# Optimization experiments

Hardware: AMD Instinct MI355X
Metric: run time of the kernel (lower is better)

Reference implementation:

```python
import jax, jax.numpy as jnp
import numpy as np

N = 50000
E = 800000
NODE_IN = 64
EDGE_IN = 8
OUT = 1
SAGE_DIMS = [(64, 64), (64, 64), (64, 32), (32, 32)]
EDGE_DIMS = [(8, 64), (64, 64), (64, 32), (32, 32)]


def setup_inputs():
    key = jax.random.key(0)
    keys = iter(jax.random.split(key, 64))
    d = {}
    d["x"] = jax.random.normal(next(keys), (N, NODE_IN), jnp.float32)
    d["dis"] = jax.random.normal(next(keys), (E, EDGE_IN), jnp.float32)
    d["edge_index"] = jax.random.randint(next(keys), (2, E), 0, N, dtype=jnp.int32)
    for i, (fi, fo) in enumerate(SAGE_DIMS):
        d[f"s{i}_wl"] = jax.random.normal(next(keys), (fi, fo), jnp.float32) / np.sqrt(fi).astype(np.float32)
        d[f"s{i}_bl"] = jnp.zeros((fo,), jnp.float32)
        d[f"s{i}_wr"] = jax.random.normal(next(keys), (fi, fo), jnp.float32) / np.sqrt(fi).astype(np.float32)
    for i, (fi, h) in enumerate(EDGE_DIMS):
        d[f"e{i}_w1"] = jax.random.normal(next(keys), (fi, 2 * h), jnp.float32) / np.sqrt(fi).astype(np.float32)
        d[f"e{i}_b1"] = jnp.zeros((2 * h,), jnp.float32)
        d[f"e{i}_w2"] = jax.random.normal(next(keys), (2 * h, h), jnp.float32) / np.sqrt(2 * h).astype(np.float32)
        d[f"e{i}_b2"] = jnp.zeros((h,), jnp.float32)
    d["fc_w"] = jax.random.normal(next(keys), (64, OUT), jnp.float32) / 8.0
    d["fc_b"] = jnp.zeros((OUT,), jnp.float32)
    return d


def _sage(x, row, col, wl, bl, wr):
    # PyG SAGEConv (aggr='mean'): lin_l(mean_{j->i} x_j) + lin_r(x_i); lin_l has bias.
    msg = x[row]  # [E, F] gather of source features
    s = jax.ops.segment_sum(msg, col, num_segments=N)
    cnt = jax.ops.segment_sum(jnp.ones((row.shape[0], 1), x.dtype), col, num_segments=N)
    mean = s / jnp.maximum(cnt, 1.0)  # isolated nodes -> 0 (matches scatter-mean)
    return mean @ wl + bl + x @ wr


def _edge_conv(dis, col, w1, b1, w2, b2):
    # EdgeOnlyConv: add_self_loops with num_nodes=E and zero edge_attr, so the
    # output has E rows; self-loop message = lin(0) = b1 and each segment t gets
    # mean = (sum_{edges->t} lin(dis) + b1) / (deg_in(t) + 1); then lin_update.
    msg = dis @ w1 + b1  # [E, 2h]
    s = jax.ops.segment_sum(msg, col, num_segments=E)
    deg = jax.ops.segment_sum(jnp.ones((col.shape[0], 1), dis.dtype), col, num_segments=E)
    aggr = (s + b1) / (deg + 1.0)
    return aggr @ w2 + b2


def _forward(x, dis, edge_index, sage_params, edge_params, fc_w, fc_b):
    row, col = edge_index[0], edge_index[1]
    h = x
    for wl, bl, wr in sage_params:
        h = jax.nn.leaky_relu(_sage(h, row, col, wl, bl, wr))
    d = dis
    for w1, b1, w2, b2 in edge_params:
        d = jax.nn.leaky_relu(_edge_conv(d, col, w1, b1, w2, b2))
    # dropout is identity at inference
    feats = jnp.concatenate([h[row] * h[col], d], axis=1)  # [E, hidden]
    return feats @ fc_w + fc_b


def reference(x, dis, edge_index, s0_wl, s0_bl, s0_wr, s1_wl, s1_bl, s1_wr, s2_wl, s2_bl, s2_wr, s3_wl, s3_bl, s3_wr, e0_w1, e0_b1, e0_w2, e0_b2, e1_w1, e1_b1, e1_w2, e1_b2, e2_w1, e2_b1, e2_w2, e2_b2, e3_w1, e3_b1, e3_w2, e3_b2, fc_w, fc_b):
    sage_params = [(s0_wl, s0_bl, s0_wr), (s1_wl, s1_bl, s1_wr), (s2_wl, s2_bl, s2_wr), (s3_wl, s3_bl, s3_wr)]
    edge_params = [(e0_w1, e0_b1, e0_w2, e0_b2), (e1_w1, e1_b1, e1_w2, e1_b2), (e2_w1, e2_b1, e2_w2, e2_b2), (e3_w1, e3_b1, e3_w2, e3_b2)]
    return _forward(x, dis, edge_index, sage_params, edge_params, fc_w, fc_b)
```

## Files before the change

kernel.cpp:

```cpp
#include <hip/hip_runtime.h>

#define LRELU(v) ((v) > 0.0f ? (v) : 0.01f * (v))

__device__ __forceinline__ unsigned short f2bf(float f) {
    union { float f; unsigned u; } c;
    c.f = f;
    return (unsigned short)((c.u + 0x7fffu + ((c.u >> 16) & 1)) >> 16);
}
__device__ __forceinline__ float bf_lo(unsigned u) {
    union { unsigned i; float f; } v;
    v.i = u << 16;
    return v.f;
}
__device__ __forceinline__ float bf_hi(unsigned u) {
    union { unsigned i; float f; } v;
    v.i = u & 0xffff0000u;
    return v.f;
}

__global__ void bucket_count_k(const int* __restrict__ col, int* __restrict__ bcnt, int E) {
    __shared__ int lcnt[512];
    int tid = threadIdx.x;
    for (int i = tid; i < 512; i += 1024) lcnt[i] = 0;
    __syncthreads();
    int base = blockIdx.x * 8192;
    for (int k = 0; k < 8; ++k) {
        int e = base + k * 1024 + tid;
        if (e < E) atomicAdd(&lcnt[col[e] >> 7], 1);
    }
    __syncthreads();
    for (int i = tid; i < 512; i += 1024) {
        int v = lcnt[i];
        if (v) atomicAdd(&bcnt[i], v);
    }
}

__global__ void bucket_scan_k(const int* __restrict__ bcnt, int* __restrict__ bbase,
                              int* __restrict__ bwp, int NBUCK, int E) {
    __shared__ int s[512];
    int tid = threadIdx.x;
    int v = (tid < NBUCK) ? bcnt[tid] : 0;
    s[tid] = v;
    __syncthreads();
    for (int off = 1; off < 512; off <<= 1) {
        int t = (tid >= off) ? s[tid - off] : 0;
        __syncthreads();
        s[tid] += t;
        __syncthreads();
    }
    if (tid < NBUCK) {
        int ex = s[tid] - v;
        bbase[tid] = ex;
        bwp[tid] = ex;
    }
    if (tid == 0) bbase[NBUCK] = E;
}

__global__ void bucket_scatter_k(const int* __restrict__ row, const int* __restrict__ col,
                                 int* __restrict__ bwp, int2* __restrict__ tmp, int E) {
    __shared__ int lcnt[512];
    __shared__ int gbase[512];
    int tid = threadIdx.x;
    for (int i = tid; i < 512; i += 1024) lcnt[i] = 0;
    __syncthreads();
    int base = blockIdx.x * 8192;
    int lpos[8], bk[8];
    for (int k = 0; k < 8; ++k) {
        int e = base + k * 1024 + tid;
        if (e < E) {
            int b = col[e] >> 7;
            bk[k] = b;
            lpos[k] = atomicAdd(&lcnt[b], 1);
        } else
            bk[k] = -1;
    }
    __syncthreads();
    for (int i = tid; i < 512; i += 1024) {
        int v = lcnt[i];
        gbase[i] = v ? atomicAdd(&bwp[i], v) : 0;
    }
    __syncthreads();
    for (int k = 0; k < 8; ++k) {
        int e = base + k * 1024 + tid;
        if (e < E) {
            int c = col[e];
            tmp[gbase[bk[k]] + lpos[k]] = make_int2(row[e], ((c & 127) << 25) | e);
        }
    }
}

__global__ void bucket_csr_k(const int2* __restrict__ tmp, const int* __restrict__ bbase,
                             int* __restrict__ rowptr, int* __restrict__ cnt,
                             int* __restrict__ rows, int* __restrict__ eids, int N, int E) {
    constexpr int CAP = 6144;
    __shared__ int2 buf[CAP];
    __shared__ int lcnt[128];
    __shared__ int sscan[128];
    __shared__ int lwp[128];
    int b = blockIdx.x;
    int tid = threadIdx.x;
    int s = bbase[b], e = bbase[b + 1];
    int sz = e - s;
    if (tid < 128) lcnt[tid] = 0;
    __syncthreads();
    for (int i = tid; i < sz; i += 256) {
        int2 v = tmp[s + i];
        if (i < CAP) buf[i] = v;
        atomicAdd(&lcnt[((unsigned)v.y) >> 25], 1);
    }
    __syncthreads();
    if (tid < 128) sscan[tid] = lcnt[tid];
    __syncthreads();
    for (int off = 1; off < 128; off <<= 1) {
        int t = (tid < 128 && tid >= off) ? sscan[tid - off] : 0;
        __syncthreads();
        if (tid < 128) sscan[tid] += t;
        __syncthreads();
    }
    if (tid < 128) {
        int ex = sscan[tid] - lcnt[tid];
        lwp[tid] = ex;
        int c = b * 128 + tid;
        if (c < N) {
            rowptr[c] = s + ex;
            cnt[c] = lcnt[tid];
            if (c == N - 1) rowptr[N] = E;
        }
    }
    __syncthreads();
    for (int i = tid; i < sz; i += 256) {
        int2 v = (i < CAP) ? buf[i] : tmp[s + i];
        int cl = ((unsigned)v.y) >> 25;
        int p = atomicAdd(&lwp[cl], 1);
        rows[s + p] = v.x;
        eids[s + p] = v.y & 0x1FFFFFF;
    }
}

template <int FIN, int FOUT, bool BFL>
__global__ void gemm2_k(const float* __restrict__ h, const float* __restrict__ wl,
                        const float* __restrict__ wr, const float* __restrict__ bl,
                        void* __restrict__ hl, float* __restrict__ hr, int N) {
    constexpr int XT = (2 * FOUT) / 4;
    constexpr int YT = 256 / XT;
    constexpr int NPT = 4;
    constexpr int NPB = YT * NPT;
    __shared__ float sw[FIN * 2 * FOUT];
    int lin = threadIdx.y * XT + threadIdx.x;
    for (int idx = lin; idx < FIN * FOUT; idx += 256) {
        int f = idx / FOUT, o = idx % FOUT;
        sw[f * 2 * FOUT + o] = wl[idx];
        sw[f * 2 * FOUT + FOUT + o] = wr[idx];
    }
    __syncthreads();
    int og = threadIdx.x * 4;
    int base = blockIdx.x * NPB + threadIdx.y * NPT;
    int ix[NPT] = {min(base + 0, N - 1), min(base + 1, N - 1), min(base + 2, N - 1),
                   min(base + 3, N - 1)};
    float4 s[NPT] = {{0.f, 0.f, 0.f, 0.f}, {0.f, 0.f, 0.f, 0.f}, {0.f, 0.f, 0.f, 0.f},
                     {0.f, 0.f, 0.f, 0.f}};
#pragma unroll 2
    for (int f = 0; f < FIN; f += 4) {
        float4 w0 = *(const float4*)&sw[(f + 0) * 2 * FOUT + og];
        float4 w1 = *(const float4*)&sw[(f + 1) * 2 * FOUT + og];
        float4 w2 = *(const float4*)&sw[(f + 2) * 2 * FOUT + og];
        float4 w3 = *(const float4*)&sw[(f + 3) * 2 * FOUT + og];
#pragma unroll
        for (int k = 0; k < NPT; ++k) {
// ... 13 lines not shown
            int i = base + k;
            if (i < N) {
                float4 r = {s[k].x + bias.x, s[k].y + bias.y, s[k].z + bias.z, s[k].w + bias.w};
                *(float4*)(hr + (size_t)i * FOUT + oo) = r;
            }
        }
    } else {
#pragma unroll
        for (int k = 0; k < NPT; ++k) {
            int i = base + k;
            if (i < N) {
                if (BFL) {
                    unsigned short* d = (unsigned short*)hl + (size_t)i * FOUT + oo;
                    *(ushort4*)d =
                        make_ushort4(f2bf(s[k].x), f2bf(s[k].y), f2bf(s[k].z), f2bf(s[k].w));
                } else {
                    *(float4*)((float*)hl + (size_t)i * FOUT + oo) = s[k];
                }
            }
        }
    }
}

__global__ void aggr_fused64_bf_k(const unsigned short* __restrict__ hlb,
                                  const float* __restrict__ hr, const int* __restrict__ rowptr,
                                  const int* __restrict__ rows, float* __restrict__ out, int N) {
    int wave = (blockIdx.x * blockDim.x + threadIdx.x) >> 6;
    int lane = threadIdx.x & 63;
    if (wave >= N) return;
    int u = lane >> 4, f4 = lane & 15;
    int s = rowptr[wave], e = rowptr[wave + 1];
    float4 a = {0.f, 0.f, 0.f, 0.f};
    int p = s + u;
    for (; p + 4 < e; p += 8) {
        int r0 = rows[p], r1 = rows[p + 4];
        uint2 v0 = ((const uint2*)(hlb + (size_t)r0 * 64))[f4];
        uint2 v1 = ((const uint2*)(hlb + (size_t)r1 * 64))[f4];
        a.x += bf_lo(v0.x) + bf_lo(v1.x);
        a.y += bf_hi(v0.x) + bf_hi(v1.x);
        a.z += bf_lo(v0.y) + bf_lo(v1.y);
        a.w += bf_hi(v0.y) + bf_hi(v1.y);
    }
    if (p < e) {
        uint2 v = ((const uint2*)(hlb + (size_t)rows[p] * 64))[f4];
        a.x += bf_lo(v.x); a.y += bf_hi(v.x); a.z += bf_lo(v.y); a.w += bf_hi(v.y);
    }
    a.x += __shfl_down(a.x, 32); a.y += __shfl_down(a.y, 32);
    a.z += __shfl_down(a.z, 32); a.w += __shfl_down(a.w, 32);
    a.x += __shfl_down(a.x, 16); a.y += __shfl_down(a.y, 16);
    a.z += __shfl_down(a.z, 16); a.w += __shfl_down(a.w, 16);
    if (lane < 16) {
        float inv = 1.0f / fmaxf((float)(e - s), 1.0f);
        float4 r = ((const float4*)(hr + (size_t)wave * 64))[f4];
        float4 o;
        o.x = LRELU(a.x * inv + r.x);
        o.y = LRELU(a.y * inv + r.y);
        o.z = LRELU(a.z * inv + r.z);
        o.w = LRELU(a.w * inv + r.w);
        ((float4*)(out + (size_t)wave * 64))[f4] = o;
    }
}

template <bool OUTBF>
__global__ void aggr_fused32_bf_k(const unsigned short* __restrict__ hlb,
                                  const float* __restrict__ hr, const int* __restrict__ rowptr,
                                  const int* __restrict__ rows, void* __restrict__ out, int N) {
    int wave = (blockIdx.x * blockDim.x + threadIdx.x) >> 6;
    int lane = threadIdx.x & 63;
    if (wave >= N) return;
    int u = lane >> 3, f4 = lane & 7;
    int s = rowptr[wave], e = rowptr[wave + 1];
    float4 a = {0.f, 0.f, 0.f, 0.f};
    int p = s + u;
    for (; p + 8 < e; p += 16) {
        int r0 = rows[p], r1 = rows[p + 8];
        uint2 v0 = ((const uint2*)(hlb + (size_t)r0 * 32))[f4];
        uint2 v1 = ((const uint2*)(hlb + (size_t)r1 * 32))[f4];
        a.x += bf_lo(v0.x) + bf_lo(v1.x);
        a.y += bf_hi(v0.x) + bf_hi(v1.x);
        a.z += bf_lo(v0.y) + bf_lo(v1.y);
        a.w += bf_hi(v0.y) + bf_hi(v1.y);
    }
    if (p < e) {
        uint2 v = ((const uint2*)(hlb + (size_t)rows[p] * 32))[f4];
        a.x += bf_lo(v.x); a.y += bf_hi(v.x); a.z += bf_lo(v.y); a.w += bf_hi(v.y);
    }
    a.x += __shfl_down(a.x, 32); a.y += __shfl_down(a.y, 32);
    a.z += __shfl_down(a.z, 32); a.w += __shfl_down(a.w, 32);
    a.x += __shfl_down(a.x, 16); a.y += __shfl_down(a.y, 16);
    a.z += __shfl_down(a.z, 16); a.w += __shfl_down(a.w, 16);
    a.x += __shfl_down(a.x, 8); a.y += __shfl_down(a.y, 8);
    a.z += __shfl_down(a.z, 8); a.w += __shfl_down(a.w, 8);
    if (lane < 8) {
        float inv = 1.0f / fmaxf((float)(e - s), 1.0f);
        const float4* hp = (const float4*)(hr + (size_t)wave * 32);
        float4 r = hp[f4];
        float4 o;
        o.x = LRELU(a.x * inv + r.x);
        o.y = LRELU(a.y * inv + r.y);
        o.z = LRELU(a.z * inv + r.z);
        o.w = LRELU(a.w * inv + r.w);
        if (OUTBF) {
            unsigned short* d = (unsigned short*)out + (size_t)wave * 32 + f4 * 4;
            *(ushort4*)d = make_ushort4(f2bf(o.x), f2bf(o.y), f2bf(o.z), f2bf(o.w));
        } else {
            ((float4*)((float*)out + (size_t)wave * 32))[f4] = o;
        }
    }
}

__global__ void edge_aggr8_k(const float* __restrict__ dis, const int* __restrict__ rowptr,
                             const int* __restrict__ eids, float* __restrict__ sd,
                             float* __restrict__ zbuf, int N) {
    int wave = (blockIdx.x * blockDim.x + threadIdx.x) >> 6;
    int lane = threadIdx.x & 63;
    if (wave >= N) return;
    zbuf[(size_t)wave * 64 + lane] = 0.0f;
    int u = lane >> 1, f4 = lane & 1;
    int s = rowptr[wave], e = rowptr[wave + 1];
    float4 a = {0.f, 0.f, 0.f, 0.f};
    for (int p = s + u; p < e; p += 32) {
        const float4* dp = (const float4*)(dis + (size_t)eids[p] * 8);
        float4 v = dp[f4];
        a.x += v.x; a.y += v.y; a.z += v.z; a.w += v.w;
    }
    for (int off = 32; off >= 2; off >>= 1) {
        a.x += __shfl_down(a.x, off); a.y += __shfl_down(a.y, off);
        a.z += __shfl_down(a.z, off); a.w += __shfl_down(a.w, off);
    }
    if (lane < 2) ((float4*)(sd + (size_t)wave * 8))[f4] = a;
}

template <int H2, int HOUT>
__device__ __forceinline__ void w12_body(const float* __restrict__ w1,
                                         const float* __restrict__ w2, float* __restrict__ out,
                                         int i, int o) {
    float s = 0.0f;
#pragma unroll
    for (int k = 0; k < H2; ++k) s += w1[i * H2 + k] * w2[k * HOUT + o];
    out[i * HOUT + o] = s;
}

__global__ void w12c_k(const float* __restrict__ w1_0, const float* __restrict__ w2_0,
                       float* __restrict__ o0, const float* __restrict__ w1_1,
                       const float* __restrict__ w2_1, float* __restrict__ o1,
                       const float* __restrict__ w1_2, const float* __restrict__ w2_2,
                       float* __restrict__ o2, const float* __restrict__ w1_3,
                       const float* __restrict__ w2_3, float* __restrict__ o3,
                       const float* __restrict__ b1_0, const float* __restrict__ b2_0,
                       const float* __restrict__ b1_1, const float* __restrict__ b2_1,
                       const float* __restrict__ b1_2, const float* __restrict__ b2_2,
                       const float* __restrict__ b1_3, const float* __restrict__ b2_3,
                       float* cbuf, int* __restrict__ bcnt) {
    int b = blockIdx.x;
    int o = threadIdx.x;
    if (b < 8) {
        if (o < 64) w12_body<128, 64>(w1_0, w2_0, o0, b, o);
    } else if (b < 72) {
        if (o < 64) w12_body<128, 64>(w1_1, w2_1, o1, b - 8, o);
    } else if (b < 136) {
        if (o < 32) w12_body<64, 32>(w1_2, w2_2, o2, b - 72, o);
    } else if (b < 168) {
        if (o < 32) w12_body<64, 32>(w1_3, w2_3, o3, b - 136, o);
    } else if (b == 168) {
        __shared__ float c1[64], c2[64], c3[32], u1[128], u2[64], u3[64];
        float t;
        if (o < 64) {
            t = 0.0f;
#pragma unroll
            for (int k = 0; k < 128; ++k) t += b1_0[k] * w2_0[k * 64 + o];
            cbuf[192 + o] = t;
            c1[o] = LRELU(t + b2_0[o]);
            cbuf[o] = c1[o];
            t = 0.0f;
#pragma unroll
            for (int k = 0; k < 128; ++k) t += b1_1[k] * w2_1[k * 64 + o];
            cbuf[256 + o] = t;
            c2[o] = LRELU(t + b2_1[o]);
            cbuf[64 + o] = c2[o];
        }
        if (o < 32) {
            t = 0.0f;
#pragma unroll
            for (int k = 0; k < 64; ++k) t += b1_2[k] * w2_2[k * 32 + o];
            cbuf[384 + o] = t;
            c3[o] = LRELU(t + b2_2[o]);
            cbuf[128 + o] = c3[o];
            t = 0.0f;
#pragma unroll
            for (int k = 0; k < 64; ++k) t += b1_3[k] * w2_3[k * 32 + o];
            cbuf[448 + o] = t;
            cbuf[160 + o] = LRELU(t + b2_3[o]);
        }
        __syncthreads();
        {
            float s = 0.0f;
#pragma unroll
            for (int f = 0; f < 64; ++f) s += c1[f] * w1_1[f * 128 + o];
            u1[o] = s;
        }
        if (o < 64) {
            float s = 0.0f;
#pragma unroll
            for (int f = 0; f < 64; ++f) s += c2[f] * w1_2[f * 64 + o];
            u2[o] = s;
            float s3 = 0.0f;
#pragma unroll
            for (int f = 0; f < 32; ++f) s3 += c3[f] * w1_3[f * 64 + o];
            u3[o] = s3;
        }
        __syncthreads();
        if (o < 64) {
            float s = cbuf[256 + o];
#pragma unroll
            for (int k = 0; k < 128; ++k) s += u1[k] * w2_1[k * 64 + o];
            cbuf[320 + o] = s;
        }
        if (o < 32) {
            float s = cbuf[384 + o];
#pragma unroll
            for (int k = 0; k < 64; ++k) s += u2[k] * w2_2[k * 32 + o];
            cbuf[416 + o] = s;
            float s3 = cbuf[448 + o];
#pragma unroll
            for (int k = 0; k < 64; ++k) s3 += u3[k] * w2_3[k * 32 + o];
            cbuf[480 + o] = s3;
        }
    } else {
        bcnt[o] = 0; bcnt[o + 128] = 0; bcnt[o + 256] = 0; bcnt[o + 384] = 0;
    }
}

template <int FIN, int FOUT>
__global__ void edge_compute_scatter_k(const float* __restrict__ sd, const int* __restrict__ cnt,
                                       const float* __restrict__ w12, const float* __restrict__ mw2,
                                       const float* __restrict__ b1w2, const float* __restrict__ b2,
                                       const float* __restrict__ cnext,
                                       const int* __restrict__ col, float* __restrict__ sdnext,
                                       int N, float* __restrict__ zbuf, int zf4) {
    constexpr int ROWS = 256 / FOUT;
    constexpr int NPT = 4;
    constexpr int NPB = ROWS * NPT;
    __shared__ float sw[FIN * FOUT];
    int lin = threadIdx.y * FOUT + threadIdx.x;
    for (int idx = lin; idx < FIN * FOUT; idx += 256) sw[idx] = w12[idx];
    __syncthreads();
    if (zf4) {
        float4 z4 = {0.f, 0.f, 0.f, 0.f};
        for (int z = blockIdx.x * 256 + lin; z < zf4; z += gridDim.x * 256)
            ((float4*)zbuf)[z] = z4;
    }
    int o = threadIdx.x;
    int base = blockIdx.x * NPB + threadIdx.y * NPT;
    int ix[NPT] = {min(base + 0, N - 1), min(base + 1, N - 1), min(base + 2, N - 1),
                   min(base + 3, N - 1)};
    float s[NPT] = {0.f, 0.f, 0.f, 0.f};
#pragma unroll 2
    for (int f = 0; f < FIN; f += 4) {
        float w0 = sw[(f + 0) * FOUT + o], w1 = sw[(f + 1) * FOUT + o];
        float w2 = sw[(f + 2) * FOUT + o], w3 = sw[(f + 3) * FOUT + o];
#pragma unroll
        for (int k = 0; k < NPT; ++k) {
// ... 25 lines not shown
    int lin = threadIdx.y * FOUT + threadIdx.x;
    for (int idx = lin; idx < FIN * FOUT; idx += 256) sw[idx] = w12[idx];
    __syncthreads();
    int o = threadIdx.x;
    int base = blockIdx.x * NPB + threadIdx.y * NPT;
    int ix[NPT] = {min(base + 0, N - 1), min(base + 1, N - 1), min(base + 2, N - 1),
                   min(base + 3, N - 1)};
    float s[NPT] = {0.f, 0.f, 0.f, 0.f};
#pragma unroll 2
    for (int f = 0; f < FIN; f += 4) {
        float w0 = sw[(f + 0) * FOUT + o], w1 = sw[(f + 1) * FOUT + o];
        float w2 = sw[(f + 2) * FOUT + o], w3 = sw[(f + 3) * FOUT + o];
#pragma unroll
        for (int k = 0; k < NPT; ++k) {
            float4 v = *(const float4*)(sd + (size_t)ix[k] * FIN + f);
            s[k] += v.x * w0 + v.y * w1 + v.z * w2 + v.w * w3;
        }
    }
    float mo = mw2[o], bo = b1w2[o], b2o = b2[o], fw = fcw[32 + o];
#pragma unroll
    for (int k = 0; k < NPT; ++k) {
        float deg = (float)cnt[ix[k]];
        float inv = 1.0f / (deg + 1.0f);
        float v = LRELU((s[k] + deg * mo + bo) * inv + b2o) * fw;
        v += __shfl_down(v, 16);
        v += __shfl_down(v, 8);
        v += __shfl_down(v, 4);
        v += __shfl_down(v, 2);
        v += __shfl_down(v, 1);
        if (o == 0 && base + k < N) ddot[base + k] = v;
    }
}

__device__ __forceinline__ float bdot8(uint4 a, uint4 b, const float* __restrict__ w) {
    return bf_lo(a.x) * bf_lo(b.x) * w[0] + bf_hi(a.x) * bf_hi(b.x) * w[1] +
           bf_lo(a.y) * bf_lo(b.y) * w[2] + bf_hi(a.y) * bf_hi(b.y) * w[3] +
           bf_lo(a.z) * bf_lo(b.z) * w[4] + bf_hi(a.z) * bf_hi(b.z) * w[5] +
           bf_lo(a.w) * bf_lo(b.w) * w[6] + bf_hi(a.w) * bf_hi(b.w) * w[7];
}

__global__ void final_k(const unsigned short* __restrict__ h3b, const float* __restrict__ ddot,
                        const float* __restrict__ c4, const int* __restrict__ row,
                        const int* __restrict__ col, const float* __restrict__ fcw,
                        const float* __restrict__ fcb, float* __restrict__ out, int E, int N) {
    __shared__ float sw[64];
    __shared__ float sc4[32];
    __shared__ float cdot_s;
    int tid = threadIdx.x;
    if (tid < 64) sw[tid] = fcw[tid];
    if (tid < 32) sc4[tid] = c4[tid];
    __syncthreads();
    if (tid == 0) {
        float cd = 0.0f;
#pragma unroll
        for (int k = 0; k < 32; ++k) cd += sc4[k] * sw[32 + k];
        cdot_s = cd;
    }
    __syncthreads();
    float fb = fcb[0];
    float cdot = cdot_s;
    int e0 = blockIdx.x * 512 + tid;
    int e1 = e0 + 256;
    bool v0 = e0 < E, v1 = e1 < E;
    int r0 = 0, c0 = 0, r1 = 0, c1 = 0;
    if (v0) { r0 = row[e0]; c0 = col[e0]; }
    if (v1) { r1 = row[e1]; c1 = col[e1]; }
    uint4 a00, a01, b00, b01, a10, a11, b10, b11;
    if (v0) {
        const uint4* pr = (const uint4*)(h3b + (size_t)r0 * 32);
        const uint4* pc = (const uint4*)(h3b + (size_t)c0 * 32);
        a00 = pr[0]; a01 = pr[1]; b00 = pc[0]; b01 = pc[1];
    }
    if (v1) {
        const uint4* pr = (const uint4*)(h3b + (size_t)r1 * 32);
        const uint4* pc = (const uint4*)(h3b + (size_t)c1 * 32);
        a10 = pr[0]; a11 = pr[1]; b10 = pc[0]; b11 = pc[1];
    }
    if (v0) {
        float s = fb + bdot8(a00, b00, sw) + bdot8(a01, b01, sw + 8) +
                  bdot8(((const uint4*)(h3b + (size_t)r0 * 32))[2],
                        ((const uint4*)(h3b + (size_t)c0 * 32))[2], sw + 16) +
                  bdot8(((const uint4*)(h3b + (size_t)r0 * 32))[3],
                        ((const uint4*)(h3b + (size_t)c0 * 32))[3], sw + 24);
        s += (e0 < N) ? ddot[e0] : cdot;
        out[e0] = s;
    }
    if (v1) {
        float s = fb + bdot8(a10, b10, sw) + bdot8(a11, b11, sw + 8) +
                  bdot8(((const uint4*)(h3b + (size_t)r1 * 32))[2],
                        ((const uint4*)(h3b + (size_t)c1 * 32))[2], sw + 16) +
                  bdot8(((const uint4*)(h3b + (size_t)r1 * 32))[3],
                        ((const uint4*)(h3b + (size_t)c1 * 32))[3], sw + 24);
        s += (e1 < N) ? ddot[e1] : cdot;
        out[e1] = s;
    }
}

extern "C" void kernel_launch(void* const* d_in, const int* in_sizes, int n_in, void* d_out,
                              int out_size, void* d_ws, size_t ws_size, hipStream_t stream) {
    const float* x = (const float*)d_in[0];
    const float* dis = (const float*)d_in[1];
    const int* ei = (const int*)d_in[2];
    const float* s_wl[4] = {(const float*)d_in[3], (const float*)d_in[6], (const float*)d_in[9],
                            (const float*)d_in[12]};
    const float* s_bl[4] = {(const float*)d_in[4], (const float*)d_in[7], (const float*)d_in[10],
                            (const float*)d_in[13]};
    const float* s_wr[4] = {(const float*)d_in[5], (const float*)d_in[8], (const float*)d_in[11],
                            (const float*)d_in[14]};
    const float* e_w1[4] = {(const float*)d_in[15], (const float*)d_in[19], (const float*)d_in[23],
                            (const float*)d_in[27]};
    const float* e_b1[4] = {(const float*)d_in[16], (const float*)d_in[20], (const float*)d_in[24],
                            (const float*)d_in[28]};
    const float* e_w2[4] = {(const float*)d_in[17], (const float*)d_in[21], (const float*)d_in[25],
                            (const float*)d_in[29]};
    const float* e_b2[4] = {(const float*)d_in[18], (const float*)d_in[22], (const float*)d_in[26],
                            (const float*)d_in[30]};
    const float* fcw = (const float*)d_in[31];
    const float* fcb = (const float*)d_in[32];

    const int N = in_sizes[0] / 64;
    const int E = in_sizes[1] / 8;
    const int* row = ei;
    const int* col = ei + E;
    const int NBUCK = (N + 127) / 128;
    const int EB = (E + 8191) / 8192;

    auto au = [](size_t v) { return (v + 255) & ~(size_t)255; };
    char* p = (char*)d_ws;
    int* cnt = (int*)p;       p += au((size_t)N * 4);
    int* rowptr = (int*)p;    p += au((size_t)(N + 1) * 4);
    int* bcnt = (int*)p;      p += au(512 * 4);
    int* bbase = (int*)p;     p += au(513 * 4);
    int* bwp = (int*)p;       p += au(512 * 4);
    float* w12_0 = (float*)p; p += au(512 * 4);
    float* w12_1 = (float*)p; p += au(4096 * 4);
    float* w12_2 = (float*)p; p += au(2048 * 4);
    float* w12_3 = (float*)p; p += au(1024 * 4);
    float* cbuf = (float*)p;  p += au(512 * 4);
    int* rowsA = (int*)p;     p += au((size_t)E * 4);
    int* eidsA = (int*)p;     p += au((size_t)E * 4);
    float* acc = (float*)p;   p += au((size_t)N * 64 * 4);
    float* hA = (float*)p;    p += au((size_t)N * 64 * 4);
    float* hB = (float*)p;    p += au((size_t)N * 64 * 4);
    float* dvA = (float*)p;   p += au((size_t)N * 64 * 4);
    float* dvB = (float*)p;   p += au((size_t)N * 64 * 4);

    int2* tmp = (int2*)dvA;
    unsigned short* hlb = (unsigned short*)acc;
    unsigned short* h3b = (unsigned short*)hA;
    float* ddot = dvB;

    w12c_k<<<170, 128, 0, stream>>>(e_w1[0], e_w2[0], w12_0, e_w1[1], e_w2[1], w12_1, e_w1[2],
                                    e_w2[2], w12_2, e_w1[3], e_w2[3], w12_3, e_b1[0], e_b2[0],
                                    e_b1[1], e_b2[1], e_b1[2], e_b2[2], e_b1[3], e_b2[3], cbuf,
                                    bcnt);

    bucket_count_k<<<EB, 1024, 0, stream>>>(col, bcnt, E);
    bucket_scan_k<<<1, 512, 0, stream>>>(bcnt, bbase, bwp, NBUCK, E);
    bucket_scatter_k<<<EB, 1024, 0, stream>>>(row, col, bwp, tmp, E);
    bucket_csr_k<<<NBUCK, 256, 0, stream>>>(tmp, bbase, rowptr, cnt, rowsA, eidsA, N, E);

    const int WPB = 4;

    gemm2_k<64, 64, true><<<(N + 31) / 32, dim3(32, 8), 0, stream>>>(x, s_wl[0], s_wr[0], s_bl[0],
                                                                     hlb, dvB, N);
    aggr_fused64_bf_k<<<(N + WPB - 1) / WPB, 256, 0, stream>>>(hlb, dvB, rowptr, rowsA, hA, N);
    gemm2_k<64, 64, true><<<(N + 31) / 32, dim3(32, 8), 0, stream>>>(hA, s_wl[1], s_wr[1], s_bl[1],
                                                                     hlb, dvB, N);
    aggr_fused64_bf_k<<<(N + WPB - 1) / WPB, 256, 0, stream>>>(hlb, dvB, rowptr, rowsA, hB, N);
    gemm2_k<64, 32, true><<<(N + 63) / 64, dim3(16, 16), 0, stream>>>(hB, s_wl[2], s_wr[2],
                                                                      s_bl[2], hlb, dvB, N);
    aggr_fused32_bf_k<false><<<(N + WPB - 1) / WPB, 256, 0, stream>>>(hlb, dvB, rowptr, rowsA, hA,
                                                                      N);
    gemm2_k<32, 32, true><<<(N + 63) / 64, dim3(16, 16), 0, stream>>>(hA, s_wl[3], s_wr[3],
                                                                      s_bl[3], hlb, dvB, N);
    aggr_fused32_bf_k<true><<<(N + WPB - 1) / WPB, 256, 0, stream>>>(hlb, dvB, rowptr, rowsA, h3b,
                                                                     N);

    edge_aggr8_k<<<(N + WPB - 1) / WPB, 256, 0, stream>>>(dis, rowptr, eidsA, hB, dvA, N);
    edge_compute_scatter_k<8, 64><<<(N + 15) / 16, dim3(64, 4), 0, stream>>>(
        hB, cnt, w12_0, cbuf + 192, cbuf + 192, e_b2[0], cbuf + 0, col, dvA, N, acc, N * 16);
    edge_compute_scatter_k<64, 64><<<(N + 15) / 16, dim3(64, 4), 0, stream>>>(
        dvA, cnt, w12_1, cbuf + 320, cbuf + 256, e_b2[1], cbuf + 64, col, acc, N, hB, N * 8);
    edge_compute_scatter_k<64, 32><<<(N + 31) / 32, dim3(32, 8), 0, stream>>>(
        acc, cnt, w12_2, cbuf + 416, cbuf + 384, e_b2[2], cbuf + 128, col, hB, N, nullptr, 0);
    edge_dot_k<<<(N + 31) / 32, dim3(32, 8), 0, stream>>>(hB, cnt, w12_3, cbuf + 480, cbuf + 448,
                                                          e_b2[3], fcw, ddot, N);

    final_k<<<(E + 511) / 512, 256, 0, stream>>>(h3b, ddot, cbuf + 160, row, col, fcw, fcb,
                                                 (float*)d_out, E, N);
}
```

Baseline: 467.2 us.

## Merge setup kernels, fuse CSR build with first GEMM, and make final pass CSR-driven

Folds the weight-precompute kernel into the bucket-count kernel, using per-block partial counts instead of global atomics. The CSR build and the first SAGE GEMM now run in one launch through a shared-memory union. The last aggregation is co-launched with the edge-feature aggregation. The final edge scoring walks the CSR per destination node, loading the destination embedding once and computing the source-side dot with the collapsed fc weights. A wider unroll is added to the 64-wide aggregation. These cut launch count and redundant gathers, but add scattered output writes in the final pass and a serial reduction in the scan.

New measurement: 477.3 us. 2.2% more time.

```diff
diff --git a/kernel.cpp b/kernel.cpp
--- a/kernel.cpp
+++ b/kernel.cpp
@@ -18,28 +18,136 @@
     return v.f;
 }
 
-__global__ void bucket_count_k(const int* __restrict__ col, int* __restrict__ bcnt, int E) {
-    __shared__ int lcnt[512];
+template <int H2, int HOUT>
+__device__ __forceinline__ void w12_body(const float* __restrict__ w1,
+                                         const float* __restrict__ w2, float* __restrict__ out,
+                                         int i, int o) {
+    float s = 0.0f;
+#pragma unroll
+    for (int k = 0; k < H2; ++k) s += w1[i * H2 + k] * w2[k * HOUT + o];
+    out[i * HOUT + o] = s;
+}
+
+__global__ void count_w12c_k(const int* __restrict__ col, int* __restrict__ bpart, int E, int EB,
+                             const float* __restrict__ w1_0, const float* __restrict__ w2_0,
+                             float* __restrict__ o0, const float* __restrict__ w1_1,
+                             const float* __restrict__ w2_1, float* __restrict__ o1,
+                             const float* __restrict__ w1_2, const float* __restrict__ w2_2,
+                             float* __restrict__ o2, const float* __restrict__ w1_3,
+                             const float* __restrict__ w2_3, float* __restrict__ o3,
+                             const float* __restrict__ b1_0, const float* __restrict__ b2_0,
+                             const float* __restrict__ b1_1, const float* __restrict__ b2_1,
+                             const float* __restrict__ b1_2, const float* __restrict__ b2_2,
+                             const float* __restrict__ b1_3, const float* __restrict__ b2_3,
+                             const float* __restrict__ fcw, float* __restrict__ cbuf) {
+    int b = blockIdx.x;
     int tid = threadIdx.x;
-    for (int i = tid; i < 512; i += 1024) lcnt[i] = 0;
-    __syncthreads();
-    int base = blockIdx.x * 8192;
-    for (int k = 0; k < 8; ++k) {
-        int e = base + k * 1024 + tid;
-        if (e < E) atomicAdd(&lcnt[col[e] >> 7], 1);
-    }
-    __syncthreads();
-    for (int i = tid; i < 512; i += 1024) {
-        int v = lcnt[i];
-        if (v) atomicAdd(&bcnt[i], v);
-    }
-}
-
-__global__ void bucket_scan_k(const int* __restrict__ bcnt, int* __restrict__ bbase,
-                              int* __restrict__ bwp, int NBUCK, int E) {
+    if (b < EB) {
+        __shared__ int lcnt[512];
+        for (int i = tid; i < 512; i += 1024) lcnt[i] = 0;
+        __syncthreads();
+        int base = b * 8192;
+        for (int k = 0; k < 8; ++k) {
+            int e = base + k * 1024 + tid;
+            if (e < E) atomicAdd(&lcnt[col[e] >> 7], 1);
+        }
+        __syncthreads();
+        for (int i = tid; i < 512; i += 1024) bpart[(size_t)b * 512 + i] = lcnt[i];
+        return;
+    }
+    int bb = b - EB;
+    int o = tid;
+    if (bb < 8) {
+        if (o < 64) w12_body<128, 64>(w1_0, w2_0, o0, bb, o);
+    } else if (bb < 72) {
+        if (o < 64) w12_body<128, 64>(w1_1, w2_1, o1, bb - 8, o);
+    } else if (bb < 136) {
+        if (o < 32) w12_body<64, 32>(w1_2, w2_2, o2, bb - 72, o);
+    } else if (bb < 168) {
+        if (o < 32) w12_body<64, 32>(w1_3, w2_3, o3, bb - 136, o);
+    } else {
+        __shared__ float c1[64], c2[64], c3[32], c4s[32], u1[128], u2[64], u3[64];
+        float t;
+        if (o < 64) {
+            t = 0.0f;
+#pragma unroll
+            for (int k = 0; k < 128; ++k) t += b1_0[k] * w2_0[k * 64 + o];
+            cbuf[192 + o] = t;
+            c1[o] = LRELU(t + b2_0[o]);
+            cbuf[o] = c1[o];
+            t = 0.0f;
+#pragma unroll
+            for (int k = 0; k < 128; ++k) t += b1_1[k] * w2_1[k * 64 + o];
+            cbuf[256 + o] = t;
+            c2[o] = LRELU(t + b2_1[o]);
+            cbuf[64 + o] = c2[o];
+        }
+        if (o < 32) {
+            t = 0.0f;
+#pragma unroll
+            for (int k = 0; k < 64; ++k) t += b1_2[k] * w2_2[k * 32 + o];
+            cbuf[384 + o] = t;
+            c3[o] = LRELU(t + b2_2[o]);
+            cbuf[128 + o] = c3[o];
+            t = 0.0f;
+#pragma unroll
+            for (int k = 0; k < 64; ++k) t += b1_3[k] * w2_3[k * 32 + o];
+            cbuf[448 + o] = t;
+            float c4v = LRELU(t + b2_3[o]);
+            cbuf[160 + o] = c4v;
+            c4s[o] = c4v;
+        }
+        __syncthreads();
+        if (o < 128) {
+            float s = 0.0f;
+#pragma unroll
+            for (int f = 0; f < 64; ++f) s += c1[f] * w1_1[f * 128 + o];
+            u1[o] = s;
+        }
+        if (o < 64) {
+            float s = 0.0f;
+#pragma unroll
+            for (int f = 0; f < 64; ++f) s += c2[f] * w1_2[f * 64 + o];
+            u2[o] = s;
+            float s3 = 0.0f;
+#pragma unroll
+            for (int f = 0; f < 32; ++f) s3 += c3[f] * w1_3[f * 64 + o];
+            u3[o] = s3;
+        }
+        __syncthreads();
+        if (o < 64) {
+            float s = cbuf[256 + o];
+#pragma unroll
+            for (int k = 0; k < 128; ++k) s += u1[k] * w2_1[k * 64 + o];
+            cbuf[320 + o] = s;
+        }
+        if (o < 32) {
+            float s = cbuf[384 + o];
+#pragma unroll
+            for (int k = 0; k < 64; ++k) s += u2[k] * w2_2[k * 32 + o];
+            cbuf[416 + o] = s;
+            float s3 = cbuf[448 + o];
+#pragma unroll
+            for (int k = 0; k < 64; ++k) s3 += u3[k] * w2_3[k * 32 + o];
+            cbuf[480 + o] = s3;
+        }
+        if (o == 0) {
+            float cd = 0.0f;
+#pragma unroll
+            for (int k = 0; k < 32; ++k) cd += c4s[k] * fcw[32 + k];
+            cbuf[512] = cd;
+        }
+    }
+}
+
+__global__ void bucket_scan_k(const int* __restrict__ bpart, int* __restrict__ bbase,
+                              int* __restrict__ bwp, int NBUCK, int E, int EB) {
     __shared__ int s[512];
     int tid = threadIdx.x;
-    int v = (tid < NBUCK) ? bcnt[tid] : 0;
+    int v = 0;
+    if (tid < NBUCK) {
+        for (int b = 0; b < EB; ++b) v += bpart[(size_t)b * 512 + tid];
+    }
     s[tid] = v;
     __syncthreads();
     for (int off = 1; off < 512; off <<= 1) {
@@ -89,51 +197,116 @@
     }
 }
 
-__global__ void bucket_csr_k(const int2* __restrict__ tmp, const int* __restrict__ bbase,
-                             int* __restrict__ rowptr, int* __restrict__ cnt,
-                             int* __restrict__ rows, int* __restrict__ eids, int N, int E) {
-    constexpr int CAP = 6144;
-    __shared__ int2 buf[CAP];
-    __shared__ int lcnt[128];
-    __shared__ int sscan[128];
-    __shared__ int lwp[128];
-    int b = blockIdx.x;
+union __align__(16) CsrGemmSM {
+    struct {
+        int2 buf[6144];
+        int lcnt[128];
+        int sscan[128];
+        int lwp[128];
+    } c;
+    float sw[64 * 128];
+};
+
+__global__ void csr_gemm0_k(const int2* __restrict__ tmp, const int* __restrict__ bbase,
+                            int* __restrict__ rowptr, int* __restrict__ cnt,
+                            int* __restrict__ rows, int* __restrict__ eids, int N, int E,
+                            int NBUCK, const float* __restrict__ h, const float* __restrict__ wl,
+                            const float* __restrict__ wr, const float* __restrict__ bl,
+                            unsigned short* __restrict__ hl, float* __restrict__ hr) {
+    __shared__ CsrGemmSM sm;
     int tid = threadIdx.x;
-    int s = bbase[b], e = bbase[b + 1];
-    int sz = e - s;
-    if (tid < 128) lcnt[tid] = 0;
+    if (blockIdx.x < NBUCK) {
+        constexpr int CAP = 6144;
+        int b = blockIdx.x;
+        int s = bbase[b], e = bbase[b + 1];
+        int sz = e - s;
+        if (tid < 128) sm.c.lcnt[tid] = 0;
+        __syncthreads();
+        for (int i = tid; i < sz; i += 256) {
+            int2 v = tmp[s + i];
+            if (i < CAP) sm.c.buf[i] = v;
+            atomicAdd(&sm.c.lcnt[((unsigned)v.y) >> 25], 1);
+        }
+        __syncthreads();
+        if (tid < 128) sm.c.sscan[tid] = sm.c.lcnt[tid];
+        __syncthreads();
+        for (int off = 1; off < 128; off <<= 1) {
+            int t = (tid < 128 && tid >= off) ? sm.c.sscan[tid - off] : 0;
+            __syncthreads();
+            if (tid < 128) sm.c.sscan[tid] += t;
+            __syncthreads();
+        }
+        if (tid < 128) {
+            int ex = sm.c.sscan[tid] - sm.c.lcnt[tid];
+            sm.c.lwp[tid] = ex;
+            int c = b * 128 + tid;
+            if (c < N) {
+                rowptr[c] = s + ex;
+                cnt[c] = sm.c.lcnt[tid];
+                if (c == N - 1) rowptr[N] = E;
+            }
+        }
+        __syncthreads();
+        for (int i = tid; i < sz; i += 256) {
+            int2 v = (i < CAP) ? sm.c.buf[i] : tmp[s + i];
+            int cl = ((unsigned)v.y) >> 25;
+            int p = atomicAdd(&sm.c.lwp[cl], 1);
+            rows[s + p] = v.x;
+            eids[s + p] = v.y & 0x1FFFFFF;
+        }
+        return;
+    }
+    float* sw = sm.sw;
+    int bx = blockIdx.x - NBUCK;
+    int tx = tid & 31, ty = tid >> 5;
+    for (int idx = tid; idx < 64 * 64; idx += 256) {
+        int f = idx >> 6, o = idx & 63;
+        sw[f * 128 + o] = wl[idx];
+        sw[f * 128 + 64 + o] = wr[idx];
+    }
     __syncthreads();
-    for (int i = tid; i < sz; i += 256) {
-        int2 v = tmp[s + i];
-        if (i < CAP) buf[i] = v;
-        atomicAdd(&lcnt[((unsigned)v.y) >> 25], 1);
-    }
-    __syncthreads();
-    if (tid < 128) sscan[tid] = lcnt[tid];
-    __syncthreads();
-    for (int off = 1; off < 128; off <<= 1) {
-        int t = (tid < 128 && tid >= off) ? sscan[tid - off] : 0;
-        __syncthreads();
-        if (tid < 128) sscan[tid] += t;
-        __syncthreads();
-    }
-    if (tid < 128) {
-        int ex = sscan[tid] - lcnt[tid];
-        lwp[tid] = ex;
-        int c = b * 128 + tid;
-        if (c < N) {
-            rowptr[c] = s + ex;
-            cnt[c] = lcnt[tid];
-            if (c == N - 1) rowptr[N] = E;
-        }
-    }
-    __syncthreads();
-    for (int i = tid; i < sz; i += 256) {
-        int2 v = (i < CAP) ? buf[i] : tmp[s + i];
-        int cl = ((unsigned)v.y) >> 25;
-        int p = atomicAdd(&lwp[cl], 1);
-        rows[s + p] = v.x;
-        eids[s + p] = v.y & 0x1FFFFFF;
+    int og = tx * 4;
+    int base = bx * 32 + ty * 4;
+    int ix[4] = {min(base + 0, N - 1), min(base + 1, N - 1), min(base + 2, N - 1),
+                 min(base + 3, N - 1)};
+    float4 s[4] = {{0.f, 0.f, 0.f, 0.f}, {0.f, 0.f, 0.f, 0.f}, {0.f, 0.f, 0.f, 0.f},
+                   {0.f, 0.f, 0.f, 0.f}};
+#pragma unroll 2
+    for (int f = 0; f < 64; f += 4) {
+        float4 w0 = *(const float4*)&sw[(f + 0) * 128 + og];
+        float4 w1 = *(const float4*)&sw[(f + 1) * 128 + og];
+        float4 w2 = *(const float4*)&sw[(f + 2) * 128 + og];
+        float4 w3 = *(const float4*)&sw[(f + 3) * 128 + og];
+#pragma unroll
+        for (int k = 0; k < 4; ++k) {
+            float4 v = *(const float4*)(h + (size_t)ix[k] * 64 + f);
+            s[k].x += v.x * w0.x + v.y * w1.x + v.z * w2.x + v.w * w3.x;
+            s[k].y += v.x * w0.y + v.y * w1.y + v.z * w2.y + v.w * w3.y;
+            s[k].z += v.x * w0.z + v.y * w1.z + v.z * w2.z + v.w * w3.z;
+            s[k].w += v.x * w0.w + v.y * w1.w + v.z * w2.w + v.w * w3.w;
+        }
+    }
+    bool isR = og >= 64;
+    int oo = isR ? og - 64 : og;
+    if (isR) {
+        float4 bias = *(const float4*)&bl[oo];
+#pragma unroll
+        for (int k = 0; k < 4; ++k) {
+            int i = base + k;
+            if (i < N) {
+                float4 r = {s[k].x + bias.x, s[k].y + bias.y, s[k].z + bias.z, s[k].w + bias.w};
+                *(float4*)(hr + (size_t)i * 64 + oo) = r;
+            }
+        }
+    } else {
+#pragma unroll
+        for (int k = 0; k < 4; ++k) {
+            int i = base + k;
+            if (i < N) {
+                unsigned short* d = hl + (size_t)i * 64 + oo;
+                *(ushort4*)d = make_ushort4(f2bf(s[k].x), f2bf(s[k].y), f2bf(s[k].z), f2bf(s[k].w));
+            }
+        }
     }
 }
 
@@ -213,6 +386,17 @@
     int s = rowptr[wave], e = rowptr[wave + 1];
     float4 a = {0.f, 0.f, 0.f, 0.f};
     int p = s + u;
+    for (; p + 12 < e; p += 16) {
+        int r0 = rows[p], r1 = rows[p + 4], r2 = rows[p + 8], r3 = rows[p + 12];
+        uint2 v0 = ((const uint2*)(hlb + (size_t)r0 * 64))[f4];
+        uint2 v1 = ((const uint2*)(hlb + (size_t)r1 * 64))[f4];
+        uint2 v2 = ((const uint2*)(hlb + (size_t)r2 * 64))[f4];
+        uint2 v3 = ((const uint2*)(hlb + (size_t)r3 * 64))[f4];
+        a.x += (bf_lo(v0.x) + bf_lo(v1.x)) + (bf_lo(v2.x) + bf_lo(v3.x));
+        a.y += (bf_hi(v0.x) + bf_hi(v1.x)) + (bf_hi(v2.x) + bf_hi(v3.x));
+        a.z += (bf_lo(v0.y) + bf_lo(v1.y)) + (bf_lo(v2.y) + bf_lo(v3.y));
+        a.w += (bf_hi(v0.y) + bf_hi(v1.y)) + (bf_hi(v2.y) + bf_hi(v3.y));
+    }
     for (; p + 4 < e; p += 8) {
         int r0 = rows[p], r1 = rows[p + 4];
         uint2 v0 = ((const uint2*)(hlb + (size_t)r0 * 64))[f4];
@@ -243,11 +427,11 @@
 }
 
 template <bool OUTBF>
-__global__ void aggr_fused32_bf_k(const unsigned short* __restrict__ hlb,
-                                  const float* __restrict__ hr, const int* __restrict__ rowptr,
-                                  const int* __restrict__ rows, void* __restrict__ out, int N) {
-    int wave = (blockIdx.x * blockDim.x + threadIdx.x) >> 6;
-    int lane = threadIdx.x & 63;
+__device__ __forceinline__ void aggr32_body(const unsigned short* __restrict__ hlb,
+                                            const float* __restrict__ hr,
+                                            const int* __restrict__ rowptr,
+                                            const int* __restrict__ rows, void* __restrict__ out,
+                                            int N, int wave, int lane) {
     if (wave >= N) return;
     int u = lane >> 3, f4 = lane & 7;
     int s = rowptr[wave], e = rowptr[wave + 1];
@@ -290,11 +474,20 @@
     }
 }
 
-__global__ void edge_aggr8_k(const float* __restrict__ dis, const int* __restrict__ rowptr,
-                             const int* __restrict__ eids, float* __restrict__ sd,
-                             float* __restrict__ zbuf, int N) {
+template <bool OUTBF>
+__global__ void aggr_fused32_bf_k(const unsigned short* __restrict__ hlb,
+                                  const float* __restrict__ hr, const int* __restrict__ rowptr,
+                                  const int* __restrict__ rows, void* __restrict__ out, int N) {
     int wave = (blockIdx.x * blockDim.x + threadIdx.x) >> 6;
     int lane = threadIdx.x & 63;
+    aggr32_body<OUTBF>(hlb, hr, rowptr, rows, out, N, wave, lane);
+}
+
+__device__ __forceinline__ void edge_aggr8_body(const float* __restrict__ dis,
+                                                const int* __restrict__ rowptr,
+                                                const int* __restrict__ eids,
+                                                float* __restrict__ sd, float* __restrict__ zbuf,
+                                                int N, int wave, int lane) {
     if (wave >= N) return;
     zbuf[(size_t)wave * 64 + lane] = 0.0f;
     int u = lane >> 1, f4 = lane & 1;
@@ -312,103 +505,18 @@
     if (lane < 2) ((float4*)(sd + (size_t)wave * 8))[f4] = a;
 }
 
-template <int H2, int HOUT>
-__device__ __forceinline__ void w12_body(const float* __restrict__ w1,
-                                         const float* __restrict__ w2, float* __restrict__ out,
-                                         int i, int o) {
-    float s = 0.0f;
-#pragma unroll
-    for (int k = 0; k < H2; ++k) s += w1[i * H2 + k] * w2[k * HOUT + o];
-    out[i * HOUT + o] = s;
-}
-
-__global__ void w12c_k(const float* __restrict__ w1_0, const float* __restrict__ w2_0,
-                       float* __restrict__ o0, const float* __restrict__ w1_1,
-                       const float* __restrict__ w2_1, float* __restrict__ o1,
-                       const float* __restrict__ w1_2, const float* __restrict__ w2_2,
-                       float* __restrict__ o2, const float* __restrict__ w1_3,
-                       const float* __restrict__ w2_3, float* __restrict__ o3,
-                       const float* __restrict__ b1_0, const float* __restrict__ b2_0,
-                       const float* __restrict__ b1_1, const float* __restrict__ b2_1,
-                       const float* __restrict__ b1_2, const float* __restrict__ b2_2,
-                       const float* __restrict__ b1_3, const float* __restrict__ b2_3,
-                       float* cbuf, int* __restrict__ bcnt) {
-    int b = blockIdx.x;
-    int o = threadIdx.x;
-    if (b < 8) {
-        if (o < 64) w12_body<128, 64>(w1_0, w2_0, o0, b, o);
-    } else if (b < 72) {
-        if (o < 64) w12_body<128, 64>(w1_1, w2_1, o1, b - 8, o);
-    } else if (b < 136) {
-        if (o < 32) w12_body<64, 32>(w1_2, w2_2, o2, b - 72, o);
-    } else if (b < 168) {
-        if (o < 32) w12_body<64, 32>(w1_3, w2_3, o3, b - 136, o);
-    } else if (b == 168) {
-        __shared__ float c1[64], c2[64], c3[32], u1[128], u2[64], u3[64];
-        float t;
-        if (o < 64) {
-            t = 0.0f;
-#pragma unroll
-            for (int k = 0; k < 128; ++k) t += b1_0[k] * w2_0[k * 64 + o];
-            cbuf[192 + o] = t;
-            c1[o] = LRELU(t + b2_0[o]);
-            cbuf[o] = c1[o];
-            t = 0.0f;
-#pragma unroll
-            for (int k = 0; k < 128; ++k) t += b1_1[k] * w2_1[k * 64 + o];
-            cbuf[256 + o] = t;
-            c2[o] = LRELU(t + b2_1[o]);
-            cbuf[64 + o] = c2[o];
-        }
-        if (o < 32) {
-            t = 0.0f;
-#pragma unroll
-            for (int k = 0; k < 64; ++k) t += b1_2[k] * w2_2[k * 32 + o];
-            cbuf[384 + o] = t;
-            c3[o] = LRELU(t + b2_2[o]);
-            cbuf[128 + o] = c3[o];
-            t = 0.0f;
-#pragma unroll
-            for (int k = 0; k < 64; ++k) t += b1_3[k] * w2_3[k * 32 + o];
-            cbuf[448 + o] = t;
-            cbuf[160 + o] = LRELU(t + b2_3[o]);
-        }
-        __syncthreads();
-        {
-            float s = 0.0f;
-#pragma unroll
-            for (int f = 0; f < 64; ++f) s += c1[f] * w1_1[f * 128 + o];
-            u1[o] = s;
-        }
-        if (o < 64) {
-            float s = 0.0f;
-#pragma unroll
-            for (int f = 0; f < 64; ++f) s += c2[f] * w1_2[f * 64 + o];
-            u2[o] = s;
-            float s3 = 0.0f;
-#pragma unroll
-            for (int f = 0; f < 32; ++f) s3 += c3[f] * w1_3[f * 64 + o];
-            u3[o] = s3;
-        }
-        __syncthreads();
-        if (o < 64) {
-            float s = cbuf[256 + o];
-#pragma unroll
-            for (int k = 0; k < 128; ++k) s += u1[k] * w2_1[k * 64 + o];
-            cbuf[320 + o] = s;
-        }
-        if (o < 32) {
-            float s = cbuf[384 + o];
-#pragma unroll
-            for (int k = 0; k < 64; ++k) s += u2[k] * w2_2[k * 32 + o];
-            cbuf[416 + o] = s;
-            float s3 = cbuf[448 + o];
-#pragma unroll
-            for (int k = 0; k < 64; ++k) s3 += u3[k] * w2_3[k * 32 + o];
-            cbuf[480 + o] = s3;
-        }
+__global__ void aggr32bf_edge_k(const unsigned short* __restrict__ hlb,
+                                const float* __restrict__ hr, const int* __restrict__ rowptr,
+                                const int* __restrict__ rows, unsigned short* __restrict__ h3b,
+                                const float* __restrict__ dis, const int* __restrict__ eids,
+                                float* __restrict__ sd, float* __restrict__ zbuf, int N, int NB) {
+    int lane = threadIdx.x & 63;
+    if (blockIdx.x < NB) {
+        int wave = (blockIdx.x * blockDim.x + threadIdx.x) >> 6;
+        aggr32_body<true>(hlb, hr, rowptr, rows, (void*)h3b, N, wave, lane);
     } else {
-        bcnt[o] = 0; bcnt[o + 128] = 0; bcnt[o + 256] = 0; bcnt[o + 384] = 0;
+        int wave = ((blockIdx.x - NB) * blockDim.x + threadIdx.x) >> 6;
+        edge_aggr8_body(dis, rowptr, eids, sd, zbuf, N, wave, lane);
     }
 }
 
@@ -500,67 +608,47 @@
     }
 }
 
-__device__ __forceinline__ float bdot8(uint4 a, uint4 b, const float* __restrict__ w) {
-    return bf_lo(a.x) * bf_lo(b.x) * w[0] + bf_hi(a.x) * bf_hi(b.x) * w[1] +
-           bf_lo(a.y) * bf_lo(b.y) * w[2] + bf_hi(a.y) * bf_hi(b.y) * w[3] +
-           bf_lo(a.z) * bf_lo(b.z) * w[4] + bf_hi(a.z) * bf_hi(b.z) * w[5] +
-           bf_lo(a.w) * bf_lo(b.w) * w[6] + bf_hi(a.w) * bf_hi(b.w) * w[7];
-}
-
-__global__ void final_k(const unsigned short* __restrict__ h3b, const float* __restrict__ ddot,
-                        const float* __restrict__ c4, const int* __restrict__ row,
-                        const int* __restrict__ col, const float* __restrict__ fcw,
-                        const float* __restrict__ fcb, float* __restrict__ out, int E, int N) {
-    __shared__ float sw[64];
-    __shared__ float sc4[32];
-    __shared__ float cdot_s;
-    int tid = threadIdx.x;
-    if (tid < 64) sw[tid] = fcw[tid];
-    if (tid < 32) sc4[tid] = c4[tid];
-    __syncthreads();
-    if (tid == 0) {
-        float cd = 0.0f;
-#pragma unroll
-        for (int k = 0; k < 32; ++k) cd += sc4[k] * sw[32 + k];
-        cdot_s = cd;
-    }
-    __syncthreads();
+__global__ void final_csr_k(const unsigned short* __restrict__ h3b,
+                            const float* __restrict__ ddot, const float* __restrict__ cbuf,
+                            const int* __restrict__ rowptr, const int* __restrict__ rows,
+                            const int* __restrict__ eids, const float* __restrict__ fcw,
+                            const float* __restrict__ fcb, float* __restrict__ out, int N) {
+    int wave = (blockIdx.x * blockDim.x + threadIdx.x) >> 6;
+    int lane = threadIdx.x & 63;
+    if (wave >= N) return;
+    int u = lane >> 3, f4 = lane & 7;
+    int s = rowptr[wave], e = rowptr[wave + 1];
+    uint2 hc = ((const uint2*)(h3b + (size_t)wave * 32))[f4];
+    float c0 = bf_lo(hc.x), c1 = bf_hi(hc.x), c2 = bf_lo(hc.y), c3 = bf_hi(hc.y);
+    float4 w = ((const float4*)fcw)[f4];
+    float wc0 = c0 * w.x, wc1 = c1 * w.y, wc2 = c2 * w.z, wc3 = c3 * w.w;
     float fb = fcb[0];
-    float cdot = cdot_s;
-    int e0 = blockIdx.x * 512 + tid;
-    int e1 = e0 + 256;
-    bool v0 = e0 < E, v1 = e1 < E;
-    int r0 = 0, c0 = 0, r1 = 0, c1 = 0;
-    if (v0) { r0 = row[e0]; c0 = col[e0]; }
-    if (v1) { r1 = row[e1]; c1 = col[e1]; }
-    uint4 a00, a01, b00, b01, a10, a11, b10, b11;
-    if (v0) {
-        const uint4* pr = (const uint4*)(h3b + (size_t)r0 * 32);
-        const uint4* pc = (const uint4*)(h3b + (size_t)c0 * 32);
-        a00 = pr[0]; a01 = pr[1]; b00 = pc[0]; b01 = pc[1];
-    }
-    if (v1) {
-        const uint4* pr = (const uint4*)(h3b + (size_t)r1 * 32);
-        const uint4* pc = (const uint4*)(h3b + (size_t)c1 * 32);
-        a10 = pr[0]; a11 = pr[1]; b10 = pc[0]; b11 = pc[1];
-    }
-    if (v0) {
-        float s = fb + bdot8(a00, b00, sw) + bdot8(a01, b01, sw + 8) +
-                  bdot8(((const uint4*)(h3b + (size_t)r0 * 32))[2],
-                        ((const uint4*)(h3b + (size_t)c0 * 32))[2], sw + 16) +
-                  bdot8(((const uint4*)(h3b + (size_t)r0 * 32))[3],
-                        ((const uint4*)(h3b + (size_t)c0 * 32))[3], sw + 24);
-        s += (e0 < N) ? ddot[e0] : cdot;
-        out[e0] = s;
-    }
-    if (v1) {
-        float s = fb + bdot8(a10, b10, sw) + bdot8(a11, b11, sw + 8) +
-                  bdot8(((const uint4*)(h3b + (size_t)r1 * 32))[2],
-                        ((const uint4*)(h3b + (size_t)c1 * 32))[2], sw + 16) +
-                  bdot8(((const uint4*)(h3b + (size_t)r1 * 32))[3],
-                        ((const uint4*)(h3b + (size_t)c1 * 32))[3], sw + 24);
-        s += (e1 < N) ? ddot[e1] : cdot;
-        out[e1] = s;
+    float cdot = cbuf[512];
+    int p = s + u;
+    for (; p + 8 < e; p += 16) {
+        int ra = rows[p], rb = rows[p + 8];
+        int ea_ = eids[p], eb_ = eids[p + 8];
+        uint2 va = ((const uint2*)(h3b + (size_t)ra * 32))[f4];
+        uint2 vb = ((const uint2*)(h3b + (size_t)rb * 32))[f4];
+        float ta = bf_lo(va.x) * wc0 + bf_hi(va.x) * wc1 + bf_lo(va.y) * wc2 + bf_hi(va.y) * wc3;
+        float tb = bf_lo(vb.x) * wc0 + bf_hi(vb.x) * wc1 + bf_lo(vb.y) * wc2 + bf_hi(vb.y) * wc3;
+        ta += __shfl_down(ta, 4); tb += __shfl_down(tb, 4);
+        ta += __shfl_down(ta, 2); tb += __shfl_down(tb, 2);
+        ta += __shfl_down(ta, 1); tb += __shfl_down(tb, 1);
+        if (f4 == 0) {
+            out[ea_] = ta + fb + (ea_ < N ? ddot[ea_] : cdot);
+            out[eb_] = tb + fb + (eb_ < N ? ddot[eb_] : cdot);
+        }
+    }
+    if (p < e) {
+        int ra = rows[p];
+        int ea_ = eids[p];
+        uint2 va = ((const uint2*)(h3b + (size_t)ra * 32))[f4];
+        float ta = bf_lo(va.x) * wc0 + bf_hi(va.x) * wc1 + bf_lo(va.y) * wc2 + bf_hi(va.y) * wc3;
+        ta += __shfl_down(ta, 4);
+        ta += __shfl_down(ta, 2);
+        ta += __shfl_down(ta, 1);
+        if (f4 == 0) out[ea_] = ta + fb + (ea_ < N ? ddot[ea_] : cdot);
     }
 }
 
@@ -597,14 +685,13 @@
     char* p = (char*)d_ws;
     int* cnt = (int*)p;       p += au((size_t)N * 4);
     int* rowptr = (int*)p;    p += au((size_t)(N + 1) * 4);
-    int* bcnt = (int*)p;      p += au(512 * 4);
     int* bbase = (int*)p;     p += au(513 * 4);
     int* bwp = (int*)p;       p += au(512 * 4);
     float* w12_0 = (float*)p; p += au(512 * 4);
     float* w12_1 = (float*)p; p += au(4096 * 4);
     float* w12_2 = (float*)p; p += au(2048 * 4);
     float* w12_3 = (float*)p; p += au(1024 * 4);
-    float* cbuf = (float*)p;  p += au(512 * 4);
+    float* cbuf = (float*)p;  p += au(544 * 4);
     int* rowsA = (int*)p;     p += au((size_t)E * 4);
     int* eidsA = (int*)p;     p += au((size_t)E * 4);
     float* acc = (float*)p;   p += au((size_t)N * 64 * 4);
@@ -614,38 +701,36 @@
     float* dvB = (float*)p;   p += au((size_t)N * 64 * 4);
 
     int2* tmp = (int2*)dvA;
+    int* bpart = (int*)hB;
     unsigned short* hlb = (unsigned short*)acc;
     unsigned short* h3b = (unsigned short*)hA;
     float* ddot = dvB;
 
-    w12c_k<<<170, 128, 0, stream>>>(e_w1[0], e_w2[0], w12_0, e_w1[1], e_w2[1], w12_1, e_w1[2],
-                                    e_w2[2], w12_2, e_w1[3], e_w2[3], w12_3, e_b1[0], e_b2[0],
-                                    e_b1[1], e_b2[1], e_b1[2], e_b2[2], e_b1[3], e_b2[3], cbuf,
-                                    bcnt);
-
-    bucket_count_k<<<EB, 1024, 0, stream>>>(col, bcnt, E);
-    bucket_scan_k<<<1, 512, 0, stream>>>(bcnt, bbase, bwp, NBUCK, E);
+    const int G0 = (N + 31) / 32;
+    const int WPB = 4;
+    const int NB = (N + WPB - 1) / WPB;
+
+    count_w12c_k<<<EB + 169, 1024, 0, stream>>>(
+        col, bpart, E, EB, e_w1[0], e_w2[0], w12_0, e_w1[1], e_w2[1], w12_1, e_w1[2], e_w2[2],
+        w12_2, e_w1[3], e_w2[3], w12_3, e_b1[0], e_b2[0], e_b1[1], e_b2[1], e_b1[2], e_b2[2],
+        e_b1[3], e_b2[3], fcw, cbuf);
+    bucket_scan_k<<<1, 512, 0, stream>>>(bpart, bbase, bwp, NBUCK, E, EB);
     bucket_scatter_k<<<EB, 1024, 0, stream>>>(row, col, bwp, tmp, E);
-    bucket_csr_k<<<NBUCK, 256, 0, stream>>>(tmp, bbase, rowptr, cnt, rowsA, eidsA, N, E);
-
-    const int WPB = 4;
-
-    gemm2_k<64, 64, true><<<(N + 31) / 32, dim3(32, 8), 0, stream>>>(x, s_wl[0], s_wr[0], s_bl[0],
-                                                                     hlb, dvB, N);
-    aggr_fused64_bf_k<<<(N + WPB - 1) / WPB, 256, 0, stream>>>(hlb, dvB, rowptr, rowsA, hA, N);
-    gemm2_k<64, 64, true><<<(N + 31) / 32, dim3(32, 8), 0, stream>>>(hA, s_wl[1], s_wr[1], s_bl[1],
-                                                                     hlb, dvB, N);
-    aggr_fused64_bf_k<<<(N + WPB - 1) / WPB, 256, 0, stream>>>(hlb, dvB, rowptr, rowsA, hB, N);
+    csr_gemm0_k<<<NBUCK + G0, 256, 0, stream>>>(tmp, bbase, rowptr, cnt, rowsA, eidsA, N, E,
+                                                NBUCK, x, s_wl[0], s_wr[0], s_bl[0], hlb, dvB);
+
+    aggr_fused64_bf_k<<<NB, 256, 0, stream>>>(hlb, dvB, rowptr, rowsA, hA, N);
+    gemm2_k<64, 64, true><<<G0, dim3(32, 8), 0, stream>>>(hA, s_wl[1], s_wr[1], s_bl[1], hlb,
+                                                          dvB, N);
+    aggr_fused64_bf_k<<<NB, 256, 0, stream>>>(hlb, dvB, rowptr, rowsA, hB, N);
     gemm2_k<64, 32, true><<<(N + 63) / 64, dim3(16, 16), 0, stream>>>(hB, s_wl[2], s_wr[2],
                                                                       s_bl[2], hlb, dvB, N);
-    aggr_fused32_bf_k<false><<<(N + WPB - 1) / WPB, 256, 0, stream>>>(hlb, dvB, rowptr, rowsA, hA,
-                                                                      N);
+    aggr_fused32_bf_k<false><<<NB, 256, 0, stream>>>(hlb, dvB, rowptr, rowsA, hA, N);
     gemm2_k<32, 32, true><<<(N + 63) / 64, dim3(16, 16), 0, stream>>>(hA, s_wl[3], s_wr[3],
                                                                       s_bl[3], hlb, dvB, N);
-    aggr_fused32_bf_k<true><<<(N + WPB - 1) / WPB, 256, 0, stream>>>(hlb, dvB, rowptr, rowsA, h3b,
-                                                                     N);
-
-    edge_aggr8_k<<<(N + WPB - 1) / WPB, 256, 0, stream>>>(dis, rowptr, eidsA, hB, dvA, N);
+    aggr32bf_edge_k<<<2 * NB, 256, 0, stream>>>(hlb, dvB, rowptr, rowsA, h3b, dis, eidsA, hB, dvA,
+                                                N, NB);
+
     edge_compute_scatter_k<8, 64><<<(N + 15) / 16, dim3(64, 4), 0, stream>>>(
         hB, cnt, w12_0, cbuf + 192, cbuf + 192, e_b2[0], cbuf + 0, col, dvA, N, acc, N * 16);
     edge_compute_scatter_k<64, 64><<<(N + 15) / 16, dim3(64, 4), 0, stream>>>(
@@ -655,6 +740,6 @@
     edge_dot_k<<<(N + 31) / 32, dim3(32, 8), 0, stream>>>(hB, cnt, w12_3, cbuf + 480, cbuf + 448,
                                                           e_b2[3], fcw, ddot, N);
 
-    final_k<<<(E + 511) / 512, 256, 0, stream>>>(h3b, ddot, cbuf + 160, row, col, fcw, fcb,
-                                                 (float*)d_out, E, N);
-}
+    final_csr_k<<<NB, 256, 0, stream>>>(h3b, ddot, cbuf, rowptr, rowsA, eidsA, fcw, fcb,
+                                        (float*)d_out, N);
+}
```
